# Performance work log

Measured on AMD Instinct MI355X. Metric: run time of the kernel, lower is better.

## Reference

```python
import jax, jax.numpy as jnp
import numpy as np

EMBED = 256
HEADS = 8
HD = EMBED // HEADS
LEVELS = 4
POINTS = 4
FFN_H = 1024
BS = 8
LQ = 900
SHAPES = [(100, 100), (50, 50), (25, 25), (13, 13)]


def setup_inputs() -> dict:
    key = jax.random.key(0)
    ks = jax.random.split(key, 20)
    nv = sum(h * w for h, w in SHAPES)
    starts = np.cumsum([0] + [h * w for h, w in SHAPES])[:-1]
    inp = {
        "queries": jax.random.normal(ks[0], (BS, LQ, EMBED), jnp.float32),
        "memory": jax.random.normal(ks[1], (BS, nv, EMBED), jnp.float32),
        "query_pos": jax.random.normal(ks[2], (BS, LQ, EMBED), jnp.float32),
        "reference_points": jax.random.uniform(ks[3], (BS, LQ, LEVELS, 4), jnp.float32) * 0.9 + 0.05,
        "spatial_shapes": jnp.asarray(SHAPES, jnp.int32),
        "level_start_index": jnp.asarray(starts, jnp.int32),
    }
    def lin(k, din, dout):
        k1, k2 = jax.random.split(k)
        w = jax.random.normal(k1, (din, dout), jnp.float32) * 0.02
        b = jax.random.normal(k2, (dout,), jnp.float32) * 0.01
        return w, b
    specs = [("Wq", "bq", EMBED, EMBED), ("Wk", "bk", EMBED, EMBED), ("Wv", "bv", EMBED, EMBED),
             ("Wo", "bo", EMBED, EMBED), ("Wvd", "bvd", EMBED, EMBED),
             ("Woff", "boff", EMBED, HEADS * LEVELS * POINTS * 2),
             ("Watt", "batt", EMBED, HEADS * LEVELS * POINTS),
             ("Wop", "bop", EMBED, EMBED), ("Wg", "bg", 2 * EMBED, 2 * EMBED),
             ("W1", "b1", EMBED, FFN_H), ("W2", "b2", FFN_H, EMBED)]
    for i, (wn, bn, di, do) in enumerate(specs):
        w, b = lin(ks[4 + i], di, do)
        inp[wn] = w
        inp[bn] = b
    for n in ["ln1", "ln2", "ln3"]:
        inp[n + "_s"] = jnp.ones((EMBED,), jnp.float32)
        inp[n + "_b"] = jnp.zeros((EMBED,), jnp.float32)
    return inp


def _ln(x, s, b):
    m = jnp.mean(x, -1, keepdims=True)
    v = jnp.mean(jnp.square(x - m), -1, keepdims=True)
    return (x - m) * jax.lax.rsqrt(v + 1e-5) * s + b


def _bilinear(v_l, lx, ly, H, W):
    # v_l: [bs,h,H*W,hd]; lx,ly: [bs,h,lq,p] normalized in [0,1]
    # grid_sample(align_corners=False, padding=zeros) semantics
    px = lx * W - 0.5
    py = ly * H - 0.5
    x0 = jnp.floor(px)
    y0 = jnp.floor(py)
    wx = px - x0
    wy = py - y0
    x0i = x0.astype(jnp.int32)
    y0i = y0.astype(jnp.int32)
    bs, h, lq, p = lx.shape
    out = jnp.zeros((bs, h, lq, p, HD), v_l.dtype)
    for dy in (0, 1):
        for dx in (0, 1):
            xi = x0i + dx
            yi = y0i + dy
            w = (wx if dx else 1.0 - wx) * (wy if dy else 1.0 - wy)
            valid = (xi >= 0) & (xi < W) & (yi >= 0) & (yi < H)
            idx = jnp.clip(yi, 0, H - 1) * W + jnp.clip(xi, 0, W - 1)
            g = jnp.take_along_axis(v_l, idx.reshape(bs, h, lq * p)[..., None], axis=2)
            g = g.reshape(bs, h, lq, p, HD)
            out = out + w[..., None] * jnp.where(valid[..., None], g, 0.0)
    return out


def reference(queries, memory, query_pos, reference_points, spatial_shapes, level_start_index,
              Wq, bq, Wk, bk, Wv, bv, Wo, bo, Wvd, bvd, Woff, boff, Watt, batt, Wop, bop,
              Wg, bg, W1, b1, W2, b2, ln1_s, ln1_b, ln2_s, ln2_b, ln3_s, ln3_b):
    bs, lq, _ = queries.shape
    shp = np.asarray(spatial_shapes)
    st = np.asarray(level_start_index)

    # ---- self attention (pre-norm, q=k=x+pos, v=x) ----
    x = _ln(queries, ln1_s, ln1_b)
    qk = x + query_pos
    Q = (qk @ Wq + bq).reshape(bs, lq, HEADS, HD)
    K = (qk @ Wk + bk).reshape(bs, lq, HEADS, HD)
    V = (x @ Wv + bv).reshape(bs, lq, HEADS, HD)
    scores = jnp.einsum('bqhd,bkhd->bhqk', Q, K) * (1.0 / np.sqrt(HD))
    attn = jax.nn.softmax(scores, axis=-1)
    sa = jnp.einsum('bhqk,bkhd->bqhd', attn, V).reshape(bs, lq, EMBED) @ Wo + bo
    x1 = queries + sa  # dropout is identity in eval

    # ---- MS-deformable cross attention ----
    y = _ln(x1, ln2_s, ln2_b)
    qc = y + query_pos
    val = (memory @ Wvd + bvd).reshape(bs, -1, HEADS, HD).transpose(0, 2, 1, 3)  # [bs,h,Nv,hd]
    off = (qc @ Woff + boff).reshape(bs, lq, HEADS, LEVELS, POINTS, 2)
    aw = jax.nn.softmax((qc @ Watt + batt).reshape(bs, lq, HEADS, LEVELS * POINTS), axis=-1)
    aw = aw.reshape(bs, lq, HEADS, LEVELS, POINTS)
    rp = reference_points[:, :, None, :, None, :]  # [bs,lq,1,L,1,4]
    loc = rp[..., :2] + off / POINTS * rp[..., 2:] * 0.5  # [bs,lq,h,L,p,2]

    out = jnp.zeros((bs, HEADS, lq, HD), queries.dtype)
    for l in range(LEVELS):
        H, W = int(shp[l, 0]), int(shp[l, 1])
        s0 = int(st[l])
        v_l = val[:, :, s0:s0 + H * W]
        lx = jnp.transpose(loc[:, :, :, l, :, 0], (0, 2, 1, 3))  # [bs,h,lq,p]
        ly = jnp.transpose(loc[:, :, :, l, :, 1], (0, 2, 1, 3))
        samp = _bilinear(v_l, lx, ly, H, W)  # [bs,h,lq,p,hd]
        w = jnp.transpose(aw[:, :, :, l], (0, 2, 1, 3))  # [bs,h,lq,p]
        out = out + jnp.sum(w[..., None] * samp, axis=3)
    cross = out.transpose(0, 2, 1, 3).reshape(bs, lq, EMBED) @ Wop + bop

    # ---- gated fusion ----
    gi = jnp.concatenate([x1, cross], axis=-1)
    g = jax.nn.sigmoid(gi @ Wg + bg)
    x2 = g[..., :EMBED] * x1 + g[..., EMBED:] * cross

    # ---- FFN ----
    z = _ln(x2, ln3_s, ln3_b)
    ffn = jax.nn.relu(z @ W1 + b1) @ W2 + b2
    return (x2 + ffn, aw, loc)
```

## Files before the change

### kernel.cpp

```cpp
#include <hip/hip_runtime.h>
#include <hip/hip_bf16.h>
#include <math.h>

#define BB 8
#define LQ 900
#define EE 256
#define NH 8
#define HD 32
#define NL 4
#define NP 4
#define FFN_H 1024

typedef __bf16 bf16x8 __attribute__((ext_vector_type(8)));
typedef float f32x4 __attribute__((ext_vector_type(4)));
typedef unsigned short u16x8 __attribute__((ext_vector_type(8)));

__device__ __forceinline__ unsigned short f2b(float f) {
    union { float f; unsigned int u; } v; v.f = f;
    unsigned int u = v.u;
    unsigned int r = (u + 0x7fffu + ((u >> 16) & 1u)) >> 16;
    return (unsigned short)r;
}
__device__ __forceinline__ float b2f(unsigned short h) {
    union { unsigned int u; float f; } v; v.u = ((unsigned int)h) << 16; return v.f;
}

typedef __attribute__((address_space(3))) unsigned int* lds_ptr_t;
typedef const __attribute__((address_space(1))) unsigned int* gbl_ptr_t;
#define GLOAD16(g, l) __builtin_amdgcn_global_load_lds((gbl_ptr_t)(g), (lds_ptr_t)(l), 16, 0, 0)
#define VMCNT(n) asm volatile("s_waitcnt vmcnt(" #n ")" ::: "memory")

struct TDesc { const float* src; unsigned short* dst; int K, N, tile0; };
struct TPack { TDesc d[11]; };

__global__ __launch_bounds__(256) void trans_kernel(TPack p) {
    int bi = blockIdx.x;
    int di = 0;
#pragma unroll
    for (int i = 1; i < 11; ++i) if (bi >= p.d[i].tile0) di = i;
    TDesc d = p.d[di];
    int t = bi - d.tile0;
    int tn = (d.N + 31) >> 5;
    int tk = t / tn, tc = t % tn;
    __shared__ float tile[32][33];
    int tx = threadIdx.x & 31, ty = threadIdx.x >> 5;
#pragma unroll
    for (int i = 0; i < 4; ++i) {
        int kk = tk * 32 + ty + i * 8, nn = tc * 32 + tx;
        tile[ty + i * 8][tx] = d.src[(size_t)kk * d.N + nn];
    }
    __syncthreads();
#pragma unroll
    for (int i = 0; i < 4; ++i) {
        int nn = tc * 32 + ty + i * 8, kk = tk * 32 + tx;
        d.dst[(size_t)nn * d.K + kk] = f2b(tile[tx][ty + i * 8]);
    }
}

__global__ void bcat_kernel(const float* __restrict__ a, const float* __restrict__ b,
                            float* __restrict__ o) {
    int t = blockIdx.x * 256 + threadIdx.x;
    if (t < 256) o[t] = a[t];
    else if (t < 512) o[t] = b[t - 256];
}

__global__ __launch_bounds__(256) void cast_kernel(const float* __restrict__ in,
                                                   unsigned short* __restrict__ out, long n) {
    long i = ((long)blockIdx.x * 256 + threadIdx.x) * 8;
    long stride = (long)gridDim.x * 256 * 8;
    for (; i < n; i += stride) {
        float4 a = *(const float4*)(in + i);
        float4 b = *(const float4*)(in + i + 4);
        u16x8 o;
        o[0] = f2b(a.x); o[1] = f2b(a.y); o[2] = f2b(a.z); o[3] = f2b(a.w);
        o[4] = f2b(b.x); o[5] = f2b(b.y); o[6] = f2b(b.z); o[7] = f2b(b.w);
        *(u16x8*)(out + i) = o;
    }
}

__global__ __launch_bounds__(256) void ln_bf(
    const float* __restrict__ in, const float* __restrict__ s,
    const float* __restrict__ b, const float* __restrict__ add,
    unsigned short* __restrict__ outx, unsigned short* __restrict__ outxa)
{
    const int row = blockIdx.x;
    const int t = threadIdx.x;
    const int w = t >> 6;
    const int lane = t & 63;
    __shared__ float red[4];

    float v = in[(size_t)row * EE + t];
    float sum = v;
#pragma unroll
    for (int o = 32; o; o >>= 1) sum += __shfl_xor(sum, o, 64);
    if (lane == 0) red[w] = sum;
    __syncthreads();
    float mean = (red[0] + red[1] + red[2] + red[3]) * (1.0f / 256.0f);
    __syncthreads();

    float d = v - mean;
    float sq = d * d;
#pragma unroll
    for (int o = 32; o; o >>= 1) sq += __shfl_xor(sq, o, 64);
    if (lane == 0) red[w] = sq;
    __syncthreads();
    float var = (red[0] + red[1] + red[2] + red[3]) * (1.0f / 256.0f);

    float y = d * rsqrtf(var + 1e-5f) * s[t] + b[t];
    if (outx)  outx[(size_t)row * EE + t] = f2b(y);
    if (outxa) outxa[(size_t)row * EE + t] = f2b(y + add[(size_t)row * EE + t]);
}

struct GD {
    const unsigned short* A;
    const unsigned short* Bt;
    const float* bias;
    const float* resid;
    float* outF;
    unsigned short* outB;
    int M, K, N, ntN, tile0, ldOutB, outBoff, act;
};
struct GB { GD d[3]; int nd, tot; };

__global__ __launch_bounds__(256, 4) void gemm_pipe(GB g) {
    __shared__ __align__(16) unsigned short ldsbuf[2][(64 + 128) * 32];
    const int tid = threadIdx.x;
    const int l = tid & 63, w = tid >> 6;
    const int wr = w >> 1, wc = w & 1;
    const int lrow = l >> 2;
    const int schunk = (((l & 3) ^ ((l >> 2) & 3)) << 4);
    const int rch = (((l >> 4) ^ (l & 3)) << 4);

    int t = blockIdx.x;
    if (t >= g.tot) return;
    int d = 0;
    while (d + 1 < g.nd && t >= g.d[d + 1].tile0) ++d;

    auto stage = [&](int dd, int tt, int ks, int pp) {
        const GD& D = g.d[dd];
        int local = tt - D.tile0;
        int m0 = (local / D.ntN) * 64;
        int n0 = (local % D.ntN) * 128;
        unsigned short* base = &ldsbuf[pp][0];
        {
            int r0 = w * 16;
            int rowg = m0 + r0 + lrow;
            int mm = D.M - 1;
            rowg = rowg < mm ? rowg : mm;
            const char* src = (const char*)(D.A + (size_t)rowg * D.K + (ks << 5)) + schunk;
            GLOAD16(src, base + r0 * 32);
        }
#pragma unroll
        for (int ib = 0; ib < 2; ++ib) {
            int r0 = ib * 64 + w * 16;
            int rowg = n0 + r0 + lrow;
            const char* src = (const char*)(D.Bt + (size_t)rowg * D.K + (ks << 5)) + schunk;
            GLOAD16(src, base + 64 * 32 + r0 * 32);
        }
    };

    stage(d, t, 0, 0);
    int p = 0;

    while (true) {
        const GD D = g.d[d];
        int local = t - D.tile0;
        int m0 = (local / D.ntN) * 64;
        int n0 = (local % D.ntN) * 128;
        int nk = D.K >> 5;

        f32x4 acc[2][4];
#pragma unroll
        for (int i = 0; i < 2; ++i)
#pragma unroll
            for (int j = 0; j < 4; ++j) acc[i][j] = (f32x4){0.f, 0.f, 0.f, 0.f};

        for (int ks = 0; ks < nk; ++ks) {
            int nt = t, nks = ks + 1, ndd = d;
            bool have = true;
            if (nks == nk) {
                nt = t + gridDim.x; nks = 0;
                if (nt >= g.tot) have = false;
                else { while (ndd + 1 < g.nd && nt >= g.d[ndd + 1].tile0) ++ndd; }
            }
            if (have) { stage(ndd, nt, nks, p ^ 1); VMCNT(3); }
            else      { VMCNT(0); }
            __builtin_amdgcn_sched_barrier(0);
            __builtin_amdgcn_s_barrier();
            __builtin_amdgcn_sched_barrier(0);

            {
                const char* base = (const char*)&ldsbuf[p][0];
                bf16x8 af[2], bfr[4];
#pragma unroll
                for (int i = 0; i < 2; ++i) {
                    int row = wr * 32 + i * 16 + (l & 15);
                    af[i] = *(const bf16x8*)(base + row * 64 + rch);
                }
#pragma unroll
                for (int j = 0; j < 4; ++j) {
                    int row = wc * 64 + j * 16 + (l & 15);
                    bfr[j] = *(const bf16x8*)(base + 4096 + row * 64 + rch);
                }
#pragma unroll
                for (int i = 0; i < 2; ++i)
#pragma unroll
                    for (int j = 0; j < 4; ++j)
                        acc[i][j] = __builtin_amdgcn_mfma_f32_16x16x32_bf16(af[i], bfr[j], acc[i][j], 0, 0, 0);
            }
            __builtin_amdgcn_sched_barrier(0);
            __builtin_amdgcn_s_barrier();
            __builtin_amdgcn_sched_barrier(0);
            p ^= 1;
        }

#pragma unroll
        for (int i = 0; i < 2; ++i) {
#pragma unroll
            for (int r = 0; r < 4; ++r) {
                int gm = m0 + wr * 32 + i * 16 + ((l >> 4) << 2) + r;
                if (gm >= D.M) continue;
#pragma unroll
                for (int j = 0; j < 4; ++j) {
                    int gn = n0 + wc * 64 + j * 16 + (l & 15);
                    float v = acc[i][j][r];
                    if (D.bias)  v += D.bias[gn];
                    if (D.resid) v += D.resid[(size_t)gm * D.N + gn];
                    if (D.act == 1)      v = fmaxf(v, 0.f);
                    else if (D.act == 2) v = 1.0f / (1.0f + __expf(-v));
                    if (D.outF) D.outF[(size_t)gm * D.N + gn] = v;
                    if (D.outB) D.outB[(size_t)gm * D.ldOutB + D.outBoff + gn] = f2b(v);
                }
            }
        }

        t += gridDim.x;
        if (t >= g.tot) break;
        while (d + 1 < g.nd && t >= g.d[d + 1].tile0) ++d;
    }
}

__global__ __launch_bounds__(256) void attn_mfma(
    const unsigned short* __restrict__ QK, const unsigned short* __restrict__ Vb,
    unsigned short* __restrict__ outB)
{
    const int qt = blockIdx.x;
    const int bh = blockIdx.y;
    const int b = bh >> 3, h = bh & 7;
    const int tid = threadIdx.x;
    const int w = tid >> 6, l = tid & 63;

    __shared__ __align__(16) unsigned short Ks[64 * 32];
    __shared__ __align__(16) unsigned short VT[32 * 64];
    __shared__ __align__(16) unsigned short Ps[4][64 * 20];

    const int qrow_w = qt * 64 + w * 16;
    int qr = qrow_w + (l & 15); qr = qr < LQ ? qr : LQ - 1;
    bf16x8 qf = *(const bf16x8*)(QK + ((size_t)(b * LQ + qr)) * 512 + h * 32 + (l >> 4) * 8);

    f32x4 acc0 = {0.f, 0.f, 0.f, 0.f}, acc1 = {0.f, 0.f, 0.f, 0.f};
    float m_run = -1e30f, l_run = 0.f;
    const float scale = 0.17677669529663689f;
    const f32x4 z4 = {0.f, 0.f, 0.f, 0.f};

    for (int kt = 0; kt < 15; ++kt) {
        __syncthreads();
        {
            int key = tid >> 2;
            int dg = (tid & 3) * 8;
            int krow = kt * 64 + key; krow = krow < LQ ? krow : LQ - 1;
            size_t base = (size_t)(b * LQ + krow);
            u16x8 kv = *(const u16x8*)(QK + base * 512 + 256 + h * 32 + dg);
            *(u16x8*)((char*)Ks + key * 64 + ((dg * 2) ^ ((key & 3) << 4))) = kv;
            u16x8 vv = *(const u16x8*)(Vb + base * 256 + h * 32 + dg);
#pragma unroll
            for (int e = 0; e < 8; ++e) {
                int dd = dg + e;
                *(unsigned short*)((char*)VT + dd * 128 + ((key * 2) ^ ((dd & 7) << 4))) = vv[e];
            }
        }
        __syncthreads();

        float p[4][4];
        float tmax = -1e30f;
#pragma unroll
        for (int m = 0; m < 4; ++m) {
            int kr = m * 16 + (l & 15);
            bf16x8 kf = *(const bf16x8*)((const char*)Ks + kr * 64 +
                        (((l >> 4) * 16) ^ ((kr & 3) << 4)));
            f32x4 sf = __builtin_amdgcn_mfma_f32_16x16x32_bf16(kf, qf, z4, 0, 0, 0);
#pragma unroll
            for (int r = 0; r < 4; ++r) {
                int key = kt * 64 + m * 16 + (l >> 4) * 4 + r;
                float sv = (key < LQ) ? sf[r] * scale : -1e30f;
                p[m][r] = sv;
                tmax = fmaxf(tmax, sv);
            }
        }
        tmax = fmaxf(tmax, __shfl_xor(tmax, 16, 64));
        tmax = fmaxf(tmax, __shfl_xor(tmax, 32, 64));
        float newm = fmaxf(m_run, tmax);
        float corr = __expf(m_run - newm);
        m_run = newm;
        float tsum = 0.f;
#pragma unroll
        for (int m = 0; m < 4; ++m)
#pragma unroll
            for (int r = 0; r < 4; ++r) {
                float e = __expf(p[m][r] - newm);
                p[m][r] = e;
                tsum += e;
            }
        tsum += __shfl_xor(tsum, 16, 64);
        tsum += __shfl_xor(tsum, 32, 64);
        l_run = l_run * corr + tsum;
        acc0 *= corr;
        acc1 *= corr;

        unsigned short* pw = &Ps[w][0];
#pragma unroll
        for (int m = 0; m < 4; ++m)
#pragma unroll
            for (int r = 0; r < 4; ++r) {
                int key = m * 16 + (l >> 4) * 4 + r;
                pw[key * 20 + (l & 15)] = f2b(p[m][r]);
            }

#pragma unroll
        for (int s = 0; s < 2; ++s) {
            union { unsigned short u[8]; bf16x8 v; } pb;
#pragma unroll
            for (int j = 0; j < 8; ++j)
                pb.u[j] = pw[(s * 32 + (l >> 4) * 8 + j) * 20 + (l & 15)];
#pragma unroll
            for (int m2 = 0; m2 < 2; ++m2) {
                int dd = m2 * 16 + (l & 15);
                bf16x8 vf = *(const bf16x8*)((const char*)VT + dd * 128 +
                            ((s * 64 + (l >> 4) * 16) ^ ((dd & 7) << 4)));
                if (m2 == 0) acc0 = __builtin_amdgcn_mfma_f32_16x16x32_bf16(vf, pb.v, acc0, 0, 0, 0);
                else         acc1 = __builtin_amdgcn_mfma_f32_16x16x32_bf16(vf, pb.v, acc1, 0, 0, 0);
            }
        }
    }

    float inv = 1.0f / l_run;
    int q = qrow_w + (l & 15);
    if (q < LQ) {
        size_t obase = ((size_t)(b * LQ + q)) * 256 + h * 32;
#pragma unroll
        for (int r = 0; r < 4; ++r) {
            int d0 = (l >> 4) * 4 + r;
            outB[obase + d0]      = f2b(acc0[r] * inv);
            outB[obase + 16 + d0] = f2b(acc1[r] * inv);
        }
    }
}

__global__ __launch_bounds__(256) void sample_fused(
    const float* __restrict__ attl, const float* __restrict__ offf,
    const float* __restrict__ refp, const unsigned short* __restrict__ val,
    const int* __restrict__ shapes, const int* __restrict__ starts,
    float* __restrict__ aw_out, float* __restrict__ loc_out,
    unsigned short* __restrict__ samp, int NV)
{
    const int row = blockIdx.x;
    const int b = row / LQ;
    const int t = threadIdx.x;
    const int h = t >> 5, d = t & 31;

    __shared__ float l_logit[128];
    __shared__ float l_aw[128];
    __shared__ float l_loc[256];
    __shared__ int l_sh[NL * 2];
    __shared__ int l_st[NL];

    if (t < 128) l_logit[t] = attl[(size_t)row * 128 + t];
    {
        float o = offf[(size_t)row * 256 + t];
        int c = t & 1;
        int lv = (t >> 3) & 3;
        float rc = refp[((size_t)row * 4 + lv) * 4 + c];
        float rs = refp[((size_t)row * 4 + lv) * 4 + 2 + c];
        float loc = rc + o * 0.125f * rs;
        l_loc[t] = loc;
        loc_out[(size_t)row * 256 + t] = loc;
    }
    if (t < NL * 2) l_sh[t] = shapes[t];
    if (t < NL) l_st[t] = starts[t];
    __syncthreads();
    if (t < 128) {
        int hh = t >> 4;
        float mx = -1e30f;
#pragma unroll
        for (int i = 0; i < 16; ++i) mx = fmaxf(mx, l_logit[hh * 16 + i]);
        float sum = 0.f;
#pragma unroll
        for (int i = 0; i < 16; ++i) sum += __expf(l_logit[hh * 16 + i] - mx);
        float aw = __expf(l_logit[t] - mx) / sum;
        l_aw[t] = aw;
        aw_out[(size_t)row * 128 + t] = aw;
    }
    __syncthreads();

    float acc = 0.f;
    const unsigned short* vb = val + (size_t)b * NV * EE + h * HD + d;

#pragma unroll
    for (int lv = 0; lv < NL; ++lv) {
        const int Hh = l_sh[lv * 2], Ww = l_sh[lv * 2 + 1];
        const int s0 = l_st[lv];
#pragma unroll
        for (int p = 0; p < NP; ++p) {
            const int base = ((h * NL + lv) * NP + p) * 2;
            float lx = l_loc[base], ly = l_loc[base + 1];
            float wgt0 = l_aw[h * 16 + lv * NP + p];
            float px = lx * (float)Ww - 0.5f;
            float py = ly * (float)Hh - 0.5f;
            float x0f = floorf(px), y0f = floorf(py);
            float wx = px - x0f, wy = py - y0f;
            int x0 = (int)x0f, y0 = (int)y0f;
#pragma unroll
            for (int dy = 0; dy < 2; ++dy) {
                int yi = y0 + dy;
                bool vy = (yi >= 0) && (yi < Hh);
                int yc = min(max(yi, 0), Hh - 1);
                float wyv = dy ? wy : 1.f - wy;
#pragma unroll
                for (int dx = 0; dx < 2; ++dx) {
                    int xi = x0 + dx;
                    bool vv = vy && (xi >= 0) && (xi < Ww);
                    int xc = min(max(xi, 0), Ww - 1);
                    float wgt = wgt0 * wyv * (dx ? wx : 1.f - wx);
                    float gv = b2f(vb[(size_t)(s0 + yc * Ww + xc) * EE]);
                    acc += vv ? wgt * gv : 0.f;
                }
            }
        }
    }
    samp[(size_t)row * EE + t] = f2b(acc);
}

__global__ __launch_bounds__(256) void gate_ln3(
    const float* __restrict__ g, const float* __restrict__ x1,
    const float* __restrict__ cross, const float* __restrict__ s,
    const float* __restrict__ bln, float* __restrict__ x2out,
    unsigned short* __restrict__ zb)
{
    const int row = blockIdx.x;
    const int t = threadIdx.x;
    const int w = t >> 6;
    const int lane = t & 63;
    __shared__ float red[4];

    float g1 = g[(size_t)row * 512 + t];
    float g2 = g[(size_t)row * 512 + 256 + t];
    float v = g1 * x1[(size_t)row * EE + t] + g2 * cross[(size_t)row * EE + t];
    x2out[(size_t)row * EE + t] = v;

    float sum = v;
#pragma unroll
    for (int o = 32; o; o >>= 1) sum += __shfl_xor(sum, o, 64);
    if (lane == 0) red[w] = sum;
    __syncthreads();
    float mean = (red[0] + red[1] + red[2] + red[3]) * (1.0f / 256.0f);
    __syncthreads();

    float d = v - mean;
    float sq = d * d;
#pragma unroll
    for (int o = 32; o; o >>= 1) sq += __shfl_xor(sq, o, 64);
    if (lane == 0) red[w] = sq;
    __syncthreads();
    float var = (red[0] + red[1] + red[2] + red[3]) * (1.0f / 256.0f);

    float y = d * rsqrtf(var + 1e-5f) * s[t] + bln[t];
    zb[(size_t)row * EE + t] = f2b(y);
}

extern "C" void kernel_launch(void* const* d_in, const int* in_sizes, int n_in,
                              void* d_out, int out_size, void* d_ws, size_t ws_size,
                              hipStream_t stream)
{
    const float* queries   = (const float*)d_in[0];
    const float* memory    = (const float*)d_in[1];
    const float* query_pos = (const float*)d_in[2];
    const float* refp      = (const float*)d_in[3];
    const int*   shapes    = (const int*)d_in[4];
    const int*   starts    = (const int*)d_in[5];
    const float* Wq  = (const float*)d_in[6],  *bq  = (const float*)d_in[7];
    const float* Wk  = (const float*)d_in[8],  *bk  = (const float*)d_in[9];
    const float* Wv  = (const float*)d_in[10], *bv  = (const float*)d_in[11];
    const float* Wo  = (const float*)d_in[12], *bo  = (const float*)d_in[13];
    const float* Wvd = (const float*)d_in[14], *bvd = (const float*)d_in[15];
    const float* Woff= (const float*)d_in[16], *boff= (const float*)d_in[17];
    const float* Watt= (const float*)d_in[18], *batt= (const float*)d_in[19];
    const float* Wop = (const float*)d_in[20], *bop = (const float*)d_in[21];
    const float* Wg  = (const float*)d_in[22], *bg  = (const float*)d_in[23];
    const float* W1  = (const float*)d_in[24], *b1  = (const float*)d_in[25];
    const float* W2  = (const float*)d_in[26], *b2  = (const float*)d_in[27];
    const float* ln1_s = (const float*)d_in[28], *ln1_b = (const float*)d_in[29];
    const float* ln2_s = (const float*)d_in[30], *ln2_b = (const float*)d_in[31];
    const float* ln3_s = (const float*)d_in[32], *ln3_b = (const float*)d_in[33];

    const int NV = in_sizes[1] / (BB * EE);
    const int Mq = BB * LQ;
    const long memN = (long)BB * NV * EE;

    char* W8 = (char*)d_ws;
    size_t off = 0;
    auto alloc = [&](size_t bytes) { char* p = W8 + off; off += (bytes + 255) & ~(size_t)255; return p; };

    unsigned short* mem_b = (unsigned short*)alloc((size_t)memN * 2);
    unsigned short* val_b = (unsigned short*)alloc((size_t)memN * 2);
    unsigned short* WtQK  = (unsigned short*)alloc(512 * 256 * 2);
    unsigned short* WtV   = (unsigned short*)alloc(256 * 256 * 2);
    unsigned short* WtO   = (unsigned short*)alloc(256 * 256 * 2);
    unsigned short* WtVD  = (unsigned short*)alloc(256 * 256 * 2);
    unsigned short* WtOFF = (unsigned short*)alloc(256 * 256 * 2);
    unsigned short* WtATT = (unsigned short*)alloc(128 * 256 * 2);
    unsigned short* WtOP  = (unsigned short*)alloc(256 * 256 * 2);
    unsigned short* WtG   = (unsigned short*)alloc(512 * 512 * 2);
    unsigned short* Wt1   = (unsigned short*)alloc(1024 * 256 * 2);
    unsigned short* Wt2   = (unsigned short*)alloc(256 * 1024 * 2);
    float*          bqk   = (float*)alloc(512 * 4);
    unsigned short* qkb   = (unsigned short*)alloc((size_t)Mq * 512 * 2);
    unsigned short* vb_buf= (unsigned short*)alloc((size_t)Mq * 256 * 2);
    unsigned short* av_buf= (unsigned short*)alloc((size_t)Mq * 256 * 2);
    float*          x1    = (float*)alloc((size_t)Mq * 256 * 4);
    unsigned short* xc_cat= (unsigned short*)alloc((size_t)Mq * 512 * 2);
    unsigned short* qc_b  = (unsigned short*)alloc((size_t)Mq * 256 * 2);
    float*          cross = (float*)alloc((size_t)Mq * 256 * 4);

    unsigned short* x_b  = (unsigned short*)cross;
    unsigned short* qk_b = x_b + (size_t)Mq * 256;
    float* off_f = (float*)qkb;
    float* attl  = (float*)vb_buf;
    unsigned short* samp_b = av_buf;
    float* gbuf = (float*)mem_b;
    float* x2   = (float*)((char*)mem_b + (size_t)Mq * 512 * 4);
    unsigned short* z_b = (unsigned short*)((char*)x2 + (size_t)Mq * 256 * 4);
    unsigned short* hidden_b = (unsigned short*)((char*)z_b + (size_t)Mq * 256 * 2);

    float* out0    = (float*)d_out;
    float* aw_out  = out0 + (size_t)Mq * 256;
    float* loc_out = aw_out + (size_t)Mq * 128;

    dim3 blk(256);

    TPack tp;
    tp.d[0]  = { Wq,   WtQK,             256, 256,    0 };
    tp.d[1]  = { Wk,   WtQK + 256 * 256, 256, 256,   64 };
    tp.d[2]  = { Wv,   WtV,              256, 256,  128 };
    tp.d[3]  = { Wo,   WtO,              256, 256,  192 };
    tp.d[4]  = { Wvd,  WtVD,             256, 256,  256 };
    tp.d[5]  = { Woff, WtOFF,            256, 256,  320 };
    tp.d[6]  = { Watt, WtATT,            256, 128,  384 };
    tp.d[7]  = { Wop,  WtOP,             256, 256,  416 };
    tp.d[8]  = { Wg,   WtG,              512, 512,  480 };
    tp.d[9]  = { W1,   Wt1,              256, 1024, 736 };
    tp.d[10] = { W2,   Wt2,             1024, 256,  992 };
    trans_kernel<<<1248, blk, 0, stream>>>(tp);
    bcat_kernel<<<2, blk, 0, stream>>>(bq, bk, bqk);
    cast_kernel<<<2048, blk, 0, stream>>>(memory, mem_b, memN);

    ln_bf<<<Mq, blk, 0, stream>>>(queries, ln1_s, ln1_b, query_pos, x_b, qk_b);

    {
        GB g; g.nd = 3;
        int ntM_val = (BB * NV + 63) / 64;
        int t0 = 0;
        g.d[0] = { mem_b, WtVD, bvd, nullptr, nullptr, val_b,  BB * NV, 256, 256, 2, t0, 256, 0, 0 };
        t0 += ntM_val * 2;
        g.d[1] = { qk_b,  WtQK, bqk, nullptr, nullptr, qkb,    Mq,      256, 512, 4, t0, 512, 0, 0 };
        t0 += 113 * 4;
        g.d[2] = { x_b,   WtV,  bv,  nullptr, nullptr, vb_buf, Mq,      256, 256, 2, t0, 256, 0, 0 };
        t0 += 113 * 2;
        g.tot = t0;
        gemm_pipe<<<1536, blk, 0, stream>>>(g);
    }

    attn_mfma<<<dim3(15, BB * NH), blk, 0, stream>>>(qkb, vb_buf, av_buf);

    {
        GB g; g.nd = 1;
        g.d[0] = { av_buf, WtO, bo, queries, x1, xc_cat, Mq, 256, 256, 2, 0, 512, 0, 0 };
        g.tot = 113 * 2;
        gemm_pipe<<<g.tot, blk, 0, stream>>>(g);
    }

    ln_bf<<<Mq, blk, 0, stream>>>(x1, ln2_s, ln2_b, query_pos, nullptr, qc_b);

    {
        GB g; g.nd = 2;
        g.d[0] = { qc_b, WtOFF, boff, nullptr, off_f, nullptr, Mq, 256, 256, 2, 0,       256, 0, 0 };
        g.d[1] = { qc_b, WtATT, batt, nullptr, attl,  nullptr, Mq, 256, 128, 1, 113 * 2, 128, 0, 0 };
        g.tot = 113 * 3;
        gemm_pipe<<<g.tot, blk, 0, stream>>>(g);
    }

    sample_fused<<<Mq, blk, 0, stream>>>(attl, off_f, refp, val_b, shapes, starts,
                                         aw_out, loc_out, samp_b, NV);

    {
        GB g; g.nd = 1;
        g.d[0] = { samp_b, WtOP, bop, nullptr, cross, xc_cat, Mq, 256, 256, 2, 0, 512, 256, 0 };
        g.tot = 113 * 2;
        gemm_pipe<<<g.tot, blk, 0, stream>>>(g);
    }

    {
        GB g; g.nd = 1;
        g.d[0] = { xc_cat, WtG, bg, nullptr, gbuf, nullptr, Mq, 512, 512, 4, 0, 512, 0, 2 };
        g.tot = 113 * 4;
        gemm_pipe<<<g.tot, blk, 0, stream>>>(g);
    }

    gate_ln3<<<Mq, blk, 0, stream>>>(gbuf, x1, cross, ln3_s, ln3_b, x2, z_b);

    {
        GB g; g.nd = 1;
        g.d[0] = { z_b, Wt1, b1, nullptr, nullptr, hidden_b, Mq, 256, 1024, 8, 0, 1024, 0, 1 };
        g.tot = 113 * 8;
        gemm_pipe<<<g.tot, blk, 0, stream>>>(g);
    }

    {
        GB g; g.nd = 1;
        g.d[0] = { hidden_b, Wt2, b2, x2, out0, nullptr, Mq, 1024, 256, 2, 0, 256, 0, 0 };
        g.tot = 113 * 2;
        gemm_pipe<<<g.tot, blk, 0, stream>>>(g);
    }
}
```

Baseline: 333.7 us.

## Fuse casts, LayerNorm and bias setup into GEMMs; widen tiles; prefetch attention K/V

Several changes land together. The memory fp32→bf16 cast moves into the value-projection GEMM, LN2 is fused into the Wo GEMM epilogue, and the offset and attention-logit GEMMs merge into one N=384 GEMM. The bias-concat kernel folds into the transpose kernel. GEMM tiles widen to 64x256 with launch bounds lowered to 2 and the persistent cross-tile pipelining dropped, and the attention kernel now register-prefetches the next K/V tile. The aim is fewer launches and less intermediate traffic, at the cost of lower occupancy and fewer blocks per GEMM.

New measurement: 395.1 us. 1.18x slower.

```diff
diff --git a/kernel.cpp b/kernel.cpp
--- a/kernel.cpp
+++ b/kernel.cpp
@@ -29,21 +29,35 @@
 typedef const __attribute__((address_space(1))) unsigned int* gbl_ptr_t;
 #define GLOAD16(g, l) __builtin_amdgcn_global_load_lds((gbl_ptr_t)(g), (lds_ptr_t)(l), 16, 0, 0)
 #define VMCNT(n) asm volatile("s_waitcnt vmcnt(" #n ")" ::: "memory")
+#define LGKM0()  asm volatile("s_waitcnt lgkmcnt(0)" ::: "memory")
 
 struct TDesc { const float* src; unsigned short* dst; int K, N, tile0; };
-struct TPack { TDesc d[11]; };
+struct TPack {
+    TDesc d[11];
+    const float *bq, *bk, *boff, *batt;
+    float *bqk, *boa;
+};
 
 __global__ __launch_bounds__(256) void trans_kernel(TPack p) {
     int bi = blockIdx.x;
+    int t = threadIdx.x;
+    if (bi >= 1248) {
+        int which = bi - 1248;
+        if (which == 0)      p.bqk[t] = p.bq[t];
+        else if (which == 1) p.bqk[256 + t] = p.bk[t];
+        else if (which == 2) p.boa[t] = p.boff[t];
+        else if (t < 128)    p.boa[256 + t] = p.batt[t];
+        return;
+    }
     int di = 0;
 #pragma unroll
     for (int i = 1; i < 11; ++i) if (bi >= p.d[i].tile0) di = i;
     TDesc d = p.d[di];
-    int t = bi - d.tile0;
+    int tt = bi - d.tile0;
     int tn = (d.N + 31) >> 5;
-    int tk = t / tn, tc = t % tn;
+    int tk = tt / tn, tc = tt % tn;
     __shared__ float tile[32][33];
-    int tx = threadIdx.x & 31, ty = threadIdx.x >> 5;
+    int tx = t & 31, ty = t >> 5;
 #pragma unroll
     for (int i = 0; i < 4; ++i) {
         int kk = tk * 32 + ty + i * 8, nn = tc * 32 + tx;
@@ -54,27 +68,6 @@
     for (int i = 0; i < 4; ++i) {
         int nn = tc * 32 + ty + i * 8, kk = tk * 32 + tx;
         d.dst[(size_t)nn * d.K + kk] = f2b(tile[tx][ty + i * 8]);
-    }
-}
-
-__global__ void bcat_kernel(const float* __restrict__ a, const float* __restrict__ b,
-                            float* __restrict__ o) {
-    int t = blockIdx.x * 256 + threadIdx.x;
-    if (t < 256) o[t] = a[t];
-    else if (t < 512) o[t] = b[t - 256];
-}
-
-__global__ __launch_bounds__(256) void cast_kernel(const float* __restrict__ in,
-                                                   unsigned short* __restrict__ out, long n) {
-    long i = ((long)blockIdx.x * 256 + threadIdx.x) * 8;
-    long stride = (long)gridDim.x * 256 * 8;
-    for (; i < n; i += stride) {
-        float4 a = *(const float4*)(in + i);
-        float4 b = *(const float4*)(in + i + 4);
-        u16x8 o;
-        o[0] = f2b(a.x); o[1] = f2b(a.y); o[2] = f2b(a.z); o[3] = f2b(a.w);
-        o[4] = f2b(b.x); o[5] = f2b(b.y); o[6] = f2b(b.z); o[7] = f2b(b.w);
-        *(u16x8*)(out + i) = o;
     }
 }
 
@@ -113,130 +106,197 @@
 
 struct GD {
     const unsigned short* A;
+    const float* Af;
     const unsigned short* Bt;
     const float* bias;
     const float* resid;
     float* outF;
     unsigned short* outB;
-    int M, K, N, ntN, tile0, ldOutB, outBoff, act;
+    const float* lnS; const float* lnB; const float* lnAdd;
+    unsigned short* lnOut;
+    int M, K, N, ntN, tile0, ldOutB, outBoff, act, aF32;
 };
-struct GB { GD d[3]; int nd, tot; };
-
-__global__ __launch_bounds__(256, 4) void gemm_pipe(GB g) {
-    __shared__ __align__(16) unsigned short ldsbuf[2][(64 + 128) * 32];
+struct GB { GD d[3]; int nd; };
+
+__global__ __launch_bounds__(256, 2) void gemm_pipe(GB g) {
+    __shared__ __align__(16) unsigned short ldsb[2][(64 + 256) * 32];
+    __shared__ float lnred[2][64][2];
     const int tid = threadIdx.x;
     const int l = tid & 63, w = tid >> 6;
     const int wr = w >> 1, wc = w & 1;
-    const int lrow = l >> 2;
-    const int schunk = (((l & 3) ^ ((l >> 2) & 3)) << 4);
-    const int rch = (((l >> 4) ^ (l & 3)) << 4);
 
     int t = blockIdx.x;
-    if (t >= g.tot) return;
-    int d = 0;
-    while (d + 1 < g.nd && t >= g.d[d + 1].tile0) ++d;
-
-    auto stage = [&](int dd, int tt, int ks, int pp) {
-        const GD& D = g.d[dd];
-        int local = tt - D.tile0;
-        int m0 = (local / D.ntN) * 64;
-        int n0 = (local % D.ntN) * 128;
-        unsigned short* base = &ldsbuf[pp][0];
-        {
-            int r0 = w * 16;
-            int rowg = m0 + r0 + lrow;
-            int mm = D.M - 1;
-            rowg = rowg < mm ? rowg : mm;
-            const char* src = (const char*)(D.A + (size_t)rowg * D.K + (ks << 5)) + schunk;
-            GLOAD16(src, base + r0 * 32);
-        }
-#pragma unroll
-        for (int ib = 0; ib < 2; ++ib) {
-            int r0 = ib * 64 + w * 16;
-            int rowg = n0 + r0 + lrow;
-            const char* src = (const char*)(D.Bt + (size_t)rowg * D.K + (ks << 5)) + schunk;
-            GLOAD16(src, base + 64 * 32 + r0 * 32);
-        }
+    int di = 0;
+    while (di + 1 < g.nd && t >= g.d[di + 1].tile0) ++di;
+    const GD D = g.d[di];
+    int local = t - D.tile0;
+    const int m0 = (local / D.ntN) * 64;
+    const int n0 = (local % D.ntN) * 256;
+    const int nk = D.K >> 5;
+
+    f32x4 acc[2][8];
+#pragma unroll
+    for (int i = 0; i < 2; ++i)
+#pragma unroll
+        for (int j = 0; j < 8; ++j) acc[i][j] = (f32x4){0.f, 0.f, 0.f, 0.f};
+
+    const int sc = tid & 3;
+    float4 fA[2];
+
+    auto stageA = [&](int ks, int pp) {
+        int row = w * 16 + (l >> 2);
+        int rg = m0 + row; int mm = D.M - 1; rg = rg < mm ? rg : mm;
+        int schunk = ((l & 3) ^ ((row >> 1) & 3)) << 4;
+        const char* src = (const char*)(D.A + (size_t)rg * D.K + (ks << 5)) + schunk;
+        GLOAD16(src, &ldsb[pp][(w * 16) * 32]);
     };
-
-    stage(d, t, 0, 0);
+    auto stageB = [&](int ks, int pp) {
+#pragma unroll
+        for (int ib = 0; ib < 4; ++ib) {
+            int row = ib * 64 + w * 16 + (l >> 2);
+            int rg = n0 + row; int nn = D.N - 1; rg = rg < nn ? rg : nn;
+            int schunk = ((l & 3) ^ ((row >> 1) & 3)) << 4;
+            const char* src = (const char*)(D.Bt + (size_t)rg * D.K + (ks << 5)) + schunk;
+            GLOAD16(src, &ldsb[pp][2048 + (ib * 64 + w * 16) * 32]);
+        }
+    };
+    auto stageAf_issue = [&](int ks) {
+        int row = tid >> 2;
+        int rg = m0 + row; int mm = D.M - 1; rg = rg < mm ? rg : mm;
+        int ck = (sc ^ ((row >> 1) & 3)) * 8;
+        const float* src = D.Af + (size_t)rg * D.K + (ks << 5) + ck;
+        fA[0] = *(const float4*)src;
+        fA[1] = *(const float4*)(src + 4);
+    };
+    auto stageAf_commit = [&](int pp) {
+        int row = tid >> 2;
+        u16x8 o;
+        o[0] = f2b(fA[0].x); o[1] = f2b(fA[0].y); o[2] = f2b(fA[0].z); o[3] = f2b(fA[0].w);
+        o[4] = f2b(fA[1].x); o[5] = f2b(fA[1].y); o[6] = f2b(fA[1].z); o[7] = f2b(fA[1].w);
+        *(u16x8*)((char*)&ldsb[pp][0] + row * 64 + sc * 16) = o;
+    };
+    auto compute = [&](int pp) {
+        const char* base = (const char*)&ldsb[pp][0];
+        const int rch = ((l >> 4) ^ ((l >> 1) & 3)) << 4;
+        bf16x8 af[2];
+#pragma unroll
+        for (int i = 0; i < 2; ++i) {
+            int row = wr * 32 + i * 16 + (l & 15);
+            af[i] = *(const bf16x8*)(base + row * 64 + rch);
+        }
+#pragma unroll
+        for (int j = 0; j < 8; ++j) {
+            int row = wc * 128 + j * 16 + (l & 15);
+            bf16x8 bfr = *(const bf16x8*)(base + 4096 + row * 64 + rch);
+#pragma unroll
+            for (int i = 0; i < 2; ++i)
+                acc[i][j] = __builtin_amdgcn_mfma_f32_16x16x32_bf16(af[i], bfr, acc[i][j], 0, 0, 0);
+        }
+    };
+
     int p = 0;
-
-    while (true) {
-        const GD D = g.d[d];
-        int local = t - D.tile0;
-        int m0 = (local / D.ntN) * 64;
-        int n0 = (local % D.ntN) * 128;
-        int nk = D.K >> 5;
-
-        f32x4 acc[2][4];
-#pragma unroll
-        for (int i = 0; i < 2; ++i)
-#pragma unroll
-            for (int j = 0; j < 4; ++j) acc[i][j] = (f32x4){0.f, 0.f, 0.f, 0.f};
-
+    if (D.aF32) {
+        stageAf_issue(0);
+        stageB(0, 0);
+        stageAf_commit(0);
+        LGKM0();
         for (int ks = 0; ks < nk; ++ks) {
-            int nt = t, nks = ks + 1, ndd = d;
-            bool have = true;
-            if (nks == nk) {
-                nt = t + gridDim.x; nks = 0;
-                if (nt >= g.tot) have = false;
-                else { while (ndd + 1 < g.nd && nt >= g.d[ndd + 1].tile0) ++ndd; }
-            }
-            if (have) { stage(ndd, nt, nks, p ^ 1); VMCNT(3); }
+            bool have = ks + 1 < nk;
+            if (have) { stageAf_issue(ks + 1); stageB(ks + 1, p ^ 1); VMCNT(6); }
             else      { VMCNT(0); }
             __builtin_amdgcn_sched_barrier(0);
             __builtin_amdgcn_s_barrier();
             __builtin_amdgcn_sched_barrier(0);
-
-            {
-                const char* base = (const char*)&ldsbuf[p][0];
-                bf16x8 af[2], bfr[4];
-#pragma unroll
-                for (int i = 0; i < 2; ++i) {
-                    int row = wr * 32 + i * 16 + (l & 15);
-                    af[i] = *(const bf16x8*)(base + row * 64 + rch);
-                }
-#pragma unroll
-                for (int j = 0; j < 4; ++j) {
-                    int row = wc * 64 + j * 16 + (l & 15);
-                    bfr[j] = *(const bf16x8*)(base + 4096 + row * 64 + rch);
-                }
-#pragma unroll
-                for (int i = 0; i < 2; ++i)
-#pragma unroll
-                    for (int j = 0; j < 4; ++j)
-                        acc[i][j] = __builtin_amdgcn_mfma_f32_16x16x32_bf16(af[i], bfr[j], acc[i][j], 0, 0, 0);
-            }
+            compute(p);
+            if (have) { stageAf_commit(p ^ 1); LGKM0(); }
             __builtin_amdgcn_sched_barrier(0);
             __builtin_amdgcn_s_barrier();
             __builtin_amdgcn_sched_barrier(0);
             p ^= 1;
         }
-
+    } else {
+        stageA(0, 0);
+        stageB(0, 0);
+        for (int ks = 0; ks < nk; ++ks) {
+            bool have = ks + 1 < nk;
+            if (have) { stageA(ks + 1, p ^ 1); stageB(ks + 1, p ^ 1); VMCNT(5); }
+            else      { VMCNT(0); }
+            __builtin_amdgcn_sched_barrier(0);
+            __builtin_amdgcn_s_barrier();
+            __builtin_amdgcn_sched_barrier(0);
+            compute(p);
+            __builtin_amdgcn_sched_barrier(0);
+            __builtin_amdgcn_s_barrier();
+            __builtin_amdgcn_sched_barrier(0);
+            p ^= 1;
+        }
+    }
+
+#pragma unroll
+    for (int i = 0; i < 2; ++i) {
+#pragma unroll
+        for (int r = 0; r < 4; ++r) {
+            int gm = m0 + wr * 32 + i * 16 + ((l >> 4) << 2) + r;
+            if (gm >= D.M) continue;
+#pragma unroll
+            for (int j = 0; j < 8; ++j) {
+                int gn = n0 + wc * 128 + j * 16 + (l & 15);
+                if (gn >= D.N) continue;
+                float v = acc[i][j][r];
+                if (D.bias)  v += D.bias[gn];
+                if (D.resid) v += D.resid[(size_t)gm * D.N + gn];
+                if (D.act == 1)      v = fmaxf(v, 0.f);
+                else if (D.act == 2) v = 1.0f / (1.0f + __expf(-v));
+                acc[i][j][r] = v;
+                if (D.outF) D.outF[(size_t)gm * D.N + gn] = v;
+                if (D.outB) D.outB[(size_t)gm * D.ldOutB + D.outBoff + gn] = f2b(v);
+            }
+        }
+    }
+
+    if (D.lnOut) {
 #pragma unroll
         for (int i = 0; i < 2; ++i) {
 #pragma unroll
             for (int r = 0; r < 4; ++r) {
-                int gm = m0 + wr * 32 + i * 16 + ((l >> 4) << 2) + r;
-                if (gm >= D.M) continue;
-#pragma unroll
-                for (int j = 0; j < 4; ++j) {
-                    int gn = n0 + wc * 64 + j * 16 + (l & 15);
+                float s1 = 0.f, s2 = 0.f;
+#pragma unroll
+                for (int j = 0; j < 8; ++j) {
                     float v = acc[i][j][r];
-                    if (D.bias)  v += D.bias[gn];
-                    if (D.resid) v += D.resid[(size_t)gm * D.N + gn];
-                    if (D.act == 1)      v = fmaxf(v, 0.f);
-                    else if (D.act == 2) v = 1.0f / (1.0f + __expf(-v));
-                    if (D.outF) D.outF[(size_t)gm * D.N + gn] = v;
-                    if (D.outB) D.outB[(size_t)gm * D.ldOutB + D.outBoff + gn] = f2b(v);
+                    s1 += v; s2 += v * v;
+                }
+#pragma unroll
+                for (int o = 1; o <= 8; o <<= 1) {
+                    s1 += __shfl_xor(s1, o, 64);
+                    s2 += __shfl_xor(s2, o, 64);
+                }
+                if ((l & 15) == 0) {
+                    int row = wr * 32 + i * 16 + ((l >> 4) << 2) + r;
+                    lnred[wc][row][0] = s1;
+                    lnred[wc][row][1] = s2;
                 }
             }
         }
-
-        t += gridDim.x;
-        if (t >= g.tot) break;
-        while (d + 1 < g.nd && t >= g.d[d + 1].tile0) ++d;
+        __syncthreads();
+#pragma unroll
+        for (int i = 0; i < 2; ++i) {
+#pragma unroll
+            for (int r = 0; r < 4; ++r) {
+                int row = wr * 32 + i * 16 + ((l >> 4) << 2) + r;
+                int gm = m0 + row;
+                if (gm >= D.M) continue;
+                float mean = (lnred[0][row][0] + lnred[1][row][0]) * (1.0f / 256.0f);
+                float msq  = (lnred[0][row][1] + lnred[1][row][1]) * (1.0f / 256.0f);
+                float rs = rsqrtf(msq - mean * mean + 1e-5f);
+#pragma unroll
+                for (int j = 0; j < 8; ++j) {
+                    int gn = wc * 128 + j * 16 + (l & 15);
+                    float y = (acc[i][j][r] - mean) * rs * D.lnS[gn] + D.lnB[gn]
+                              + D.lnAdd[(size_t)gm * 256 + gn];
+                    D.lnOut[(size_t)gm * 256 + gn] = f2b(y);
+                }
+            }
+        }
     }
 }
 
@@ -263,21 +323,29 @@
     const float scale = 0.17677669529663689f;
     const f32x4 z4 = {0.f, 0.f, 0.f, 0.f};
 
+    const int key = tid >> 2;
+    const int dg = (tid & 3) * 8;
+    u16x8 kvc, vvc, kvn, vvn;
+    {
+        int krow = key; krow = krow < LQ ? krow : LQ - 1;
+        size_t base = (size_t)(b * LQ + krow);
+        kvc = *(const u16x8*)(QK + base * 512 + 256 + h * 32 + dg);
+        vvc = *(const u16x8*)(Vb + base * 256 + h * 32 + dg);
+    }
+
     for (int kt = 0; kt < 15; ++kt) {
         __syncthreads();
-        {
-            int key = tid >> 2;
-            int dg = (tid & 3) * 8;
-            int krow = kt * 64 + key; krow = krow < LQ ? krow : LQ - 1;
+        *(u16x8*)((char*)Ks + key * 64 + ((dg * 2) ^ ((key & 3) << 4))) = kvc;
+#pragma unroll
+        for (int e = 0; e < 8; ++e) {
+            int dd = dg + e;
+            *(unsigned short*)((char*)VT + dd * 128 + ((key * 2) ^ ((dd & 7) << 4))) = vvc[e];
+        }
+        if (kt < 14) {
+            int krow = (kt + 1) * 64 + key; krow = krow < LQ ? krow : LQ - 1;
             size_t base = (size_t)(b * LQ + krow);
-            u16x8 kv = *(const u16x8*)(QK + base * 512 + 256 + h * 32 + dg);
-            *(u16x8*)((char*)Ks + key * 64 + ((dg * 2) ^ ((key & 3) << 4))) = kv;
-            u16x8 vv = *(const u16x8*)(Vb + base * 256 + h * 32 + dg);
-#pragma unroll
-            for (int e = 0; e < 8; ++e) {
-                int dd = dg + e;
-                *(unsigned short*)((char*)VT + dd * 128 + ((key * 2) ^ ((dd & 7) << 4))) = vv[e];
-            }
+            kvn = *(const u16x8*)(QK + base * 512 + 256 + h * 32 + dg);
+            vvn = *(const u16x8*)(Vb + base * 256 + h * 32 + dg);
         }
         __syncthreads();
 
@@ -291,8 +359,8 @@
             f32x4 sf = __builtin_amdgcn_mfma_f32_16x16x32_bf16(kf, qf, z4, 0, 0, 0);
 #pragma unroll
             for (int r = 0; r < 4; ++r) {
-                int key = kt * 64 + m * 16 + (l >> 4) * 4 + r;
-                float sv = (key < LQ) ? sf[r] * scale : -1e30f;
+                int kk = kt * 64 + m * 16 + (l >> 4) * 4 + r;
+                float sv = (kk < LQ) ? sf[r] * scale : -1e30f;
                 p[m][r] = sv;
                 tmax = fmaxf(tmax, sv);
             }
@@ -322,8 +390,8 @@
         for (int m = 0; m < 4; ++m)
 #pragma unroll
             for (int r = 0; r < 4; ++r) {
-                int key = m * 16 + (l >> 4) * 4 + r;
-                pw[key * 20 + (l & 15)] = f2b(p[m][r]);
+                int kk = m * 16 + (l >> 4) * 4 + r;
+                pw[kk * 20 + (l & 15)] = f2b(p[m][r]);
             }
 
 #pragma unroll
@@ -341,6 +409,7 @@
                 else         acc1 = __builtin_amdgcn_mfma_f32_16x16x32_bf16(vf, pb.v, acc1, 0, 0, 0);
             }
         }
+        if (kt < 14) { kvc = kvn; vvc = vvn; }
     }
 
     float inv = 1.0f / l_run;
@@ -357,8 +426,8 @@
 }
 
 __global__ __launch_bounds__(256) void sample_fused(
-    const float* __restrict__ attl, const float* __restrict__ offf,
-    const float* __restrict__ refp, const unsigned short* __restrict__ val,
+    const float* __restrict__ off_att, const float* __restrict__ refp,
+    const unsigned short* __restrict__ val,
     const int* __restrict__ shapes, const int* __restrict__ starts,
     float* __restrict__ aw_out, float* __restrict__ loc_out,
     unsigned short* __restrict__ samp, int NV)
@@ -374,9 +443,9 @@
     __shared__ int l_sh[NL * 2];
     __shared__ int l_st[NL];
 
-    if (t < 128) l_logit[t] = attl[(size_t)row * 128 + t];
-    {
-        float o = offf[(size_t)row * 256 + t];
+    if (t < 128) l_logit[t] = off_att[(size_t)row * 384 + 256 + t];
+    {
+        float o = off_att[(size_t)row * 384 + t];
         int c = t & 1;
         int lv = (t >> 3) & 3;
         float rc = refp[((size_t)row * 4 + lv) * 4 + c];
@@ -504,48 +573,49 @@
 
     const int NV = in_sizes[1] / (BB * EE);
     const int Mq = BB * LQ;
-    const long memN = (long)BB * NV * EE;
+    const int Mv = BB * NV;
+    const long memN = (long)Mv * EE;
 
     char* W8 = (char*)d_ws;
     size_t off = 0;
     auto alloc = [&](size_t bytes) { char* p = W8 + off; off += (bytes + 255) & ~(size_t)255; return p; };
 
-    unsigned short* mem_b = (unsigned short*)alloc((size_t)memN * 2);
     unsigned short* val_b = (unsigned short*)alloc((size_t)memN * 2);
     unsigned short* WtQK  = (unsigned short*)alloc(512 * 256 * 2);
     unsigned short* WtV   = (unsigned short*)alloc(256 * 256 * 2);
     unsigned short* WtO   = (unsigned short*)alloc(256 * 256 * 2);
     unsigned short* WtVD  = (unsigned short*)alloc(256 * 256 * 2);
-    unsigned short* WtOFF = (unsigned short*)alloc(256 * 256 * 2);
-    unsigned short* WtATT = (unsigned short*)alloc(128 * 256 * 2);
+    unsigned short* WtOA  = (unsigned short*)alloc(384 * 256 * 2);
     unsigned short* WtOP  = (unsigned short*)alloc(256 * 256 * 2);
     unsigned short* WtG   = (unsigned short*)alloc(512 * 512 * 2);
     unsigned short* Wt1   = (unsigned short*)alloc(1024 * 256 * 2);
     unsigned short* Wt2   = (unsigned short*)alloc(256 * 1024 * 2);
     float*          bqk   = (float*)alloc(512 * 4);
+    float*          boa   = (float*)alloc(384 * 4);
     unsigned short* qkb   = (unsigned short*)alloc((size_t)Mq * 512 * 2);
     unsigned short* vb_buf= (unsigned short*)alloc((size_t)Mq * 256 * 2);
     unsigned short* av_buf= (unsigned short*)alloc((size_t)Mq * 256 * 2);
     float*          x1    = (float*)alloc((size_t)Mq * 256 * 4);
     unsigned short* xc_cat= (unsigned short*)alloc((size_t)Mq * 512 * 2);
     unsigned short* qc_b  = (unsigned short*)alloc((size_t)Mq * 256 * 2);
+    float*          off_att=(float*)alloc((size_t)Mq * 384 * 4);
     float*          cross = (float*)alloc((size_t)Mq * 256 * 4);
+    float*          gbuf  = (float*)alloc((size_t)Mq * 512 * 4);
+    float*          x2    = (float*)alloc((size_t)Mq * 256 * 4);
+    unsigned short* z_b   = (unsigned short*)alloc((size_t)Mq * 256 * 2);
+    unsigned short* hidden_b = (unsigned short*)alloc((size_t)Mq * 1024 * 2);
 
     unsigned short* x_b  = (unsigned short*)cross;
-    unsigned short* qk_b = x_b + (size_t)Mq * 256;
-    float* off_f = (float*)qkb;
-    float* attl  = (float*)vb_buf;
+    unsigned short* qk_b = (unsigned short*)off_att;
     unsigned short* samp_b = av_buf;
-    float* gbuf = (float*)mem_b;
-    float* x2   = (float*)((char*)mem_b + (size_t)Mq * 512 * 4);
-    unsigned short* z_b = (unsigned short*)((char*)x2 + (size_t)Mq * 256 * 4);
-    unsigned short* hidden_b = (unsigned short*)((char*)z_b + (size_t)Mq * 256 * 2);
 
     float* out0    = (float*)d_out;
     float* aw_out  = out0 + (size_t)Mq * 256;
     float* loc_out = aw_out + (size_t)Mq * 128;
 
     dim3 blk(256);
+    const int tMq = (Mq + 63) / 64;
+    const int tv  = (Mv + 63) / 64;
 
     TPack tp;
     tp.d[0]  = { Wq,   WtQK,             256, 256,    0 };
@@ -553,81 +623,84 @@
     tp.d[2]  = { Wv,   WtV,              256, 256,  128 };
     tp.d[3]  = { Wo,   WtO,              256, 256,  192 };
     tp.d[4]  = { Wvd,  WtVD,             256, 256,  256 };
-    tp.d[5]  = { Woff, WtOFF,            256, 256,  320 };
-    tp.d[6]  = { Watt, WtATT,            256, 128,  384 };
+    tp.d[5]  = { Woff, WtOA,             256, 256,  320 };
+    tp.d[6]  = { Watt, WtOA + 256 * 256, 256, 128,  384 };
     tp.d[7]  = { Wop,  WtOP,             256, 256,  416 };
     tp.d[8]  = { Wg,   WtG,              512, 512,  480 };
     tp.d[9]  = { W1,   Wt1,              256, 1024, 736 };
     tp.d[10] = { W2,   Wt2,             1024, 256,  992 };
-    trans_kernel<<<1248, blk, 0, stream>>>(tp);
-    bcat_kernel<<<2, blk, 0, stream>>>(bq, bk, bqk);
-    cast_kernel<<<2048, blk, 0, stream>>>(memory, mem_b, memN);
+    tp.bq = bq; tp.bk = bk; tp.boff = boff; tp.batt = batt;
+    tp.bqk = bqk; tp.boa = boa;
+    trans_kernel<<<1252, blk, 0, stream>>>(tp);
 
     ln_bf<<<Mq, blk, 0, stream>>>(queries, ln1_s, ln1_b, query_pos, x_b, qk_b);
 
     {
         GB g; g.nd = 3;
-        int ntM_val = (BB * NV + 63) / 64;
-        int t0 = 0;
-        g.d[0] = { mem_b, WtVD, bvd, nullptr, nullptr, val_b,  BB * NV, 256, 256, 2, t0, 256, 0, 0 };
-        t0 += ntM_val * 2;
-        g.d[1] = { qk_b,  WtQK, bqk, nullptr, nullptr, qkb,    Mq,      256, 512, 4, t0, 512, 0, 0 };
-        t0 += 113 * 4;
-        g.d[2] = { x_b,   WtV,  bv,  nullptr, nullptr, vb_buf, Mq,      256, 256, 2, t0, 256, 0, 0 };
-        t0 += 113 * 2;
-        g.tot = t0;
-        gemm_pipe<<<1536, blk, 0, stream>>>(g);
+        g.d[0] = { nullptr, memory, WtVD, bvd, nullptr, nullptr, val_b,
+                   nullptr, nullptr, nullptr, nullptr,
+                   Mv, 256, 256, 1, 0, 256, 0, 0, 1 };
+        g.d[1] = { qk_b, nullptr, WtQK, bqk, nullptr, nullptr, qkb,
+                   nullptr, nullptr, nullptr, nullptr,
+                   Mq, 256, 512, 2, tv, 512, 0, 0, 0 };
+        g.d[2] = { x_b, nullptr, WtV, bv, nullptr, nullptr, vb_buf,
+                   nullptr, nullptr, nullptr, nullptr,
+                   Mq, 256, 256, 1, tv + tMq * 2, 256, 0, 0, 0 };
+        gemm_pipe<<<tv + tMq * 3, blk, 0, stream>>>(g);
     }
 
     attn_mfma<<<dim3(15, BB * NH), blk, 0, stream>>>(qkb, vb_buf, av_buf);
 
     {
         GB g; g.nd = 1;
-        g.d[0] = { av_buf, WtO, bo, queries, x1, xc_cat, Mq, 256, 256, 2, 0, 512, 0, 0 };
-        g.tot = 113 * 2;
-        gemm_pipe<<<g.tot, blk, 0, stream>>>(g);
-    }
-
-    ln_bf<<<Mq, blk, 0, stream>>>(x1, ln2_s, ln2_b, query_pos, nullptr, qc_b);
-
-    {
-        GB g; g.nd = 2;
-        g.d[0] = { qc_b, WtOFF, boff, nullptr, off_f, nullptr, Mq, 256, 256, 2, 0,       256, 0, 0 };
-        g.d[1] = { qc_b, WtATT, batt, nullptr, attl,  nullptr, Mq, 256, 128, 1, 113 * 2, 128, 0, 0 };
-        g.tot = 113 * 3;
-        gemm_pipe<<<g.tot, blk, 0, stream>>>(g);
-    }
-
-    sample_fused<<<Mq, blk, 0, stream>>>(attl, off_f, refp, val_b, shapes, starts,
+        g.d[0] = { av_buf, nullptr, WtO, bo, queries, x1, xc_cat,
+                   ln2_s, ln2_b, query_pos, qc_b,
+                   Mq, 256, 256, 1, 0, 512, 0, 0, 0 };
+        gemm_pipe<<<tMq, blk, 0, stream>>>(g);
+    }
+
+    {
+        GB g; g.nd = 1;
+        g.d[0] = { qc_b, nullptr, WtOA, boa, nullptr, off_att, nullptr,
+                   nullptr, nullptr, nullptr, nullptr,
+                   Mq, 256, 384, 2, 0, 384, 0, 0, 0 };
+        gemm_pipe<<<tMq * 2, blk, 0, stream>>>(g);
+    }
+
+    sample_fused<<<Mq, blk, 0, stream>>>(off_att, refp, val_b, shapes, starts,
                                          aw_out, loc_out, samp_b, NV);
 
     {
         GB g; g.nd = 1;
-        g.d[0] = { samp_b, WtOP, bop, nullptr, cross, xc_cat, Mq, 256, 256, 2, 0, 512, 256, 0 };
-        g.tot = 113 * 2;
-        gemm_pipe<<<g.tot, blk, 0, stream>>>(g);
+        g.d[0] = { samp_b, nullptr, WtOP, bop, nullptr, cross, xc_cat,
+                   nullptr, nullptr, nullptr, nullptr,
+                   Mq, 256, 256, 1, 0, 512, 256, 0, 0 };
+        gemm_pipe<<<tMq, blk, 0, stream>>>(g);
     }
 
     {
         GB g; g.nd = 1;
-        g.d[0] = { xc_cat, WtG, bg, nullptr, gbuf, nullptr, Mq, 512, 512, 4, 0, 512, 0, 2 };
-        g.tot = 113 * 4;
-        gemm_pipe<<<g.tot, blk, 0, stream>>>(g);
+        g.d[0] = { xc_cat, nullptr, WtG, bg, nullptr, gbuf, nullptr,
+                   nullptr, nullptr, nullptr, nullptr,
+                   Mq, 512, 512, 2, 0, 512, 0, 2, 0 };
+        gemm_pipe<<<tMq * 2, blk, 0, stream>>>(g);
     }
 
     gate_ln3<<<Mq, blk, 0, stream>>>(gbuf, x1, cross, ln3_s, ln3_b, x2, z_b);
 
     {
         GB g; g.nd = 1;
-        g.d[0] = { z_b, Wt1, b1, nullptr, nullptr, hidden_b, Mq, 256, 1024, 8, 0, 1024, 0, 1 };
-        g.tot = 113 * 8;
-        gemm_pipe<<<g.tot, blk, 0, stream>>>(g);
+        g.d[0] = { z_b, nullptr, Wt1, b1, nullptr, nullptr, hidden_b,
+                   nullptr, nullptr, nullptr, nullptr,
+                   Mq, 256, 1024, 4, 0, 1024, 0, 1, 0 };
+        gemm_pipe<<<tMq * 4, blk, 0, stream>>>(g);
     }
 
     {
         GB g; g.nd = 1;
-        g.d[0] = { hidden_b, Wt2, b2, x2, out0, nullptr, Mq, 1024, 256, 2, 0, 256, 0, 0 };
-        g.tot = 113 * 2;
-        gemm_pipe<<<g.tot, blk, 0, stream>>>(g);
-    }
-}
+        g.d[0] = { hidden_b, nullptr, Wt2, b2, x2, out0, nullptr,
+                   nullptr, nullptr, nullptr, nullptr,
+                   Mq, 1024, 256, 1, 0, 256, 0, 0, 0 };
+        gemm_pipe<<<tMq, blk, 0, stream>>>(g);
+    }
+}
```
